# Kernel optimization log

Measured on AMD Instinct MI355X. Metric: run time of the kernel, lower is better.

The kernel has to match this reference:

```python
import jax, jax.numpy as jnp
import numpy as np

EMBED_DIM = 1024
NUM_HEADS = 16
HEAD_DIM = EMBED_DIM // NUM_HEADS
T_Q = 2048
T_K = 2048
B = 4
NEG_INF = -1e9


def setup_inputs() -> dict:
    key = jax.random.key(0)
    ks = jax.random.split(key, 8)
    q = jax.random.normal(ks[0], (T_Q, B, EMBED_DIM), dtype=jnp.float32)
    k = jax.random.normal(ks[1], (T_K, B, EMBED_DIM), dtype=jnp.float32)
    v = jax.random.normal(ks[2], (T_K, B, EMBED_DIM), dtype=jnp.float32)
    # True = padded key position (masked out)
    key_padding_mask = jax.random.randint(ks[3], (B, T_K), 0, 2).astype(jnp.bool_)
    # torch nn.Linear weights: shape (out, in), y = x @ W^T
    scale = 1.0 / np.sqrt(EMBED_DIM)
    Wq = jax.random.uniform(ks[4], (EMBED_DIM, EMBED_DIM), jnp.float32, -scale, scale)
    Wk = jax.random.uniform(ks[5], (EMBED_DIM, EMBED_DIM), jnp.float32, -scale, scale)
    Wv = jax.random.uniform(ks[6], (EMBED_DIM, EMBED_DIM), jnp.float32, -scale, scale)
    Wo = jax.random.uniform(ks[7], (EMBED_DIM, EMBED_DIM), jnp.float32, -scale, scale)
    return {"q": q, "k": k, "v": v, "key_padding_mask": key_padding_mask,
            "Wq": Wq, "Wk": Wk, "Wv": Wv, "Wo": Wo}


def _proj_split(W, x):
    # x: (T, B, E), W: (E, E) torch layout -> (B, H, T, d_k)
    T = x.shape[0]
    y = jnp.einsum('tbe,fe->tbf', x, W)
    return y.reshape(T, B, NUM_HEADS, HEAD_DIM).transpose(1, 2, 0, 3)


def reference(q, k, v, key_padding_mask, Wq, Wk, Wv, Wo):
    Q = _proj_split(Wq, q)  # (B, H, T_q, d_k)
    K = _proj_split(Wk, k)  # (B, H, T_k, d_k)
    V = _proj_split(Wv, v)  # (B, H, T_k, d_k)
    scores = jnp.einsum('bhqd,bhkd->bhqk', Q, K) / jnp.sqrt(
        jnp.asarray(HEAD_DIM, dtype=Q.dtype))
    scores = jnp.where(key_padding_mask[:, None, None, :], NEG_INF, scores)
    attn = jax.nn.softmax(scores, axis=-1)  # dropout p=0.0 -> identity
    out = jnp.einsum('bhqk,bhkd->bhqd', attn, V)  # (B, H, T_q, d_k)
    out = out.transpose(2, 0, 1, 3).reshape(q.shape[0], q.shape[1], EMBED_DIM)
    return jnp.einsum('tbe,fe->tbf', out, Wo)
```

## Files before the change

### kernel.cpp

```cpp
#include <hip/hip_runtime.h>
#include <stdint.h>

#define TSEQ 2048
#define NB   4
#define NH   16
#define HD   64
#define EMB  1024
#define ROWS (TSEQ*NB)
#define NKT  (EMB/64)
#define PREP_BLOCKS 28672

typedef __attribute__((ext_vector_type(8))) short bf16x8;
typedef __attribute__((ext_vector_type(4))) short bf16x4;
typedef __attribute__((ext_vector_type(4))) float f32x4;

__device__ __forceinline__ short f2bf(float x) {
    uint32_t u = __builtin_bit_cast(uint32_t, x);
    u += 0x7fffu + ((u >> 16) & 1u);
    return (short)(u >> 16);
}

__device__ __forceinline__ uint32_t pack2bf(float a, float b) {
    uint32_t ua = __builtin_bit_cast(uint32_t, a) + 0x8000u;
    uint32_t ub = __builtin_bit_cast(uint32_t, b) + 0x8000u;
    return (ua >> 16) | (ub & 0xffff0000u);
}

__device__ __forceinline__ void gld16(const void* g, void* l) {
    __builtin_amdgcn_global_load_lds(
        (const __attribute__((address_space(1))) void*)g,
        (__attribute__((address_space(3))) void*)l,
        16, 0, 0);
}

__global__ __launch_bounds__(256)
void prep_scan(const float* __restrict__ q, const float* __restrict__ k, const float* __restrict__ v,
               const float* __restrict__ Wq, const float* __restrict__ Wk,
               const float* __restrict__ Wv, const float* __restrict__ Wo,
               short* __restrict__ Wbf,
               short* __restrict__ Xq, short* __restrict__ Xk, short* __restrict__ Xv,
               const int* __restrict__ mask, int* __restrict__ idxc, int* __restrict__ inv,
               float* __restrict__ bias_c, int* __restrict__ npad)
{
    __shared__ int sums[256];
    __shared__ int totalv;
    const int bid = blockIdx.x, tid = threadIdx.x;

    if (bid < PREP_BLOCKS) {
        int gid = bid * 256 + tid;
        const float4* s4;
        bf16x4* d4;
        if (gid < (1 << 20)) {
            int wsel = gid >> 18;
            const float* src = (wsel == 0) ? Wq : (wsel == 1) ? Wk : (wsel == 2) ? Wv : Wo;
            s4 = (const float4*)src + (gid & ((1 << 18) - 1));
            d4 = (bf16x4*)Wbf + gid;
        } else {
            int iid = gid - (1 << 20);
            int isel = iid >> 21, o = iid & ((1 << 21) - 1);
            const float* src = (isel == 0) ? q : (isel == 1) ? k : v;
            short* dst = (isel == 0) ? Xq : (isel == 1) ? Xk : Xv;
            s4 = (const float4*)src + o;
            d4 = (bf16x4*)dst + o;
        }
        float4 vv = *s4;
        bf16x4 o4 = { f2bf(vv.x), f2bf(vv.y), f2bf(vv.z), f2bf(vv.w) };
        *d4 = o4;
        return;
    }

    const int b = bid - PREP_BLOCKS;
    const int* mb = mask + b * TSEQ;
    int valid[8]; int cnt = 0;
    #pragma unroll
    for (int j = 0; j < 8; j++) { valid[j] = (mb[tid * 8 + j] == 0); cnt += valid[j]; }
    sums[tid] = cnt;
    __syncthreads();
    for (int off = 1; off < 256; off <<= 1) {
        int vv = (tid >= off) ? sums[tid - off] : 0;
        __syncthreads();
        sums[tid] += vv;
        __syncthreads();
    }
    if (tid == 255) totalv = sums[255];
    int base = sums[tid] - cnt;
    __syncthreads();
    int nv = totalv;
    #pragma unroll
    for (int j = 0; j < 8; j++) {
        int t = tid * 8 + j;
        if (valid[j]) { idxc[b * TSEQ + base] = t; inv[b * TSEQ + t] = base; base++; }
        else          { inv[b * TSEQ + t] = -1; }
    }
    for (int i = tid; i < TSEQ; i += 256) {
        if (i >= nv) idxc[b * TSEQ + i] = 0;
        bias_c[b * TSEQ + i] = (i < nv) ? -12.0f : -1e9f;
    }
    if (tid == 0) npad[b] = (nv + 63) & ~63;
}


#define DSA(MH)                                                                     \
    _Pragma("unroll")                                                               \
    for (int mf = 0; mf < 4; mf++) {                                                \
        _Pragma("unroll")                                                           \
        for (int ks = 0; ks < 2; ks++) {                                            \
            const int rr = wm*64 + mf*16 + c;                                       \
            const int cb = (ks*64 + g*16) ^ ((rr & 7) << 4);                        \
            af[mf][ks] = *(const bf16x8*)(&lds[cur][0][MH][0] + rr*64 + (cb >> 1)); \
        }                                                                           \
    }

#define DSB(NH_, DST)                                                               \
    _Pragma("unroll")                                                               \
    for (int nf = 0; nf < 2; nf++) {                                                \
        _Pragma("unroll")                                                           \
        for (int ks = 0; ks < 2; ks++) {                                            \
            const int rr = wn*32 + nf*16 + c;                                       \
            const int cb = (ks*64 + g*16) ^ ((rr & 7) << 4);                        \
            DST[nf][ks] = *(const bf16x8*)(&lds[cur][1][NH_][0] + rr*64 + (cb >> 1));\
        }                                                                           \
    }

#define MM(MH, NH_, BREG)                                                           \
    __builtin_amdgcn_s_barrier();                                                   \
    asm volatile("s_waitcnt lgkmcnt(0)" ::: "memory");                              \
    __builtin_amdgcn_sched_barrier(0);                                              \
    __builtin_amdgcn_s_setprio(1);                                                  \
    _Pragma("unroll")                                                               \
    for (int mf = 0; mf < 4; mf++) {                                                \
        _Pragma("unroll")                                                           \
        for (int nf = 0; nf < 2; nf++) {                                            \
            acc[MH][NH_][mf][nf] = __builtin_amdgcn_mfma_f32_16x16x32_bf16(         \
                af[mf][0], BREG[nf][0], acc[MH][NH_][mf][nf], 0, 0, 0);             \
            acc[MH][NH_][mf][nf] = __builtin_amdgcn_mfma_f32_16x16x32_bf16(         \
                af[mf][1], BREG[nf][1], acc[MH][NH_][mf][nf], 0, 0, 0);             \
        }                                                                           \
    }                                                                               \
    __builtin_amdgcn_s_setprio(0);                                                  \
    __builtin_amdgcn_sched_barrier(0);

__global__ __launch_bounds__(512, 2)
void proj_gemm8(const short* __restrict__ Xq, const short* __restrict__ Xk, const short* __restrict__ Xv,
                const short* __restrict__ Wbf, const int* __restrict__ inv,
                short* __restrict__ Qw, short* __restrict__ Kc, short* __restrict__ Vw)
{
    __shared__ __align__(16) short lds[2][2][2][128*64];
    const int z = blockIdx.z;
    const short* __restrict__ A  = (z == 0) ? Xq : (z == 1) ? Xk : Xv;
    const short* __restrict__ Bw = Wbf + (size_t)z * (EMB*EMB);
    short* __restrict__ dst = (z == 0) ? Qw : (z == 1) ? Kc : Vw;
    const float scale = (z == 0) ? 0.18033688011112042f : 1.0f;

    const int tid = threadIdx.x;
    const int lane = tid & 63, w = tid >> 6;
    const int wm = w >> 2, wn = w & 3;
    const int g = lane >> 4, c = lane & 15;
    const int m0 = blockIdx.x * 256, n0 = blockIdx.y * 256;

    const short* a0 = A  + (size_t)m0 * EMB;
    const short* a1 = a0 + (size_t)128 * EMB;
    const short* b0 = Bw + (size_t)n0 * EMB;
    const short* b1 = b0 + (size_t)128 * EMB;

    auto stage = [&](const short* grow, short* lhalf) {
        #pragma unroll
        for (int p = 0; p < 2; p++) {
            const int lin = p * 8192 + w * 1024 + lane * 16;
            const int rin = lin >> 7;
            const int cb  = (lin & 127) ^ ((rin & 7) << 4);
            gld16(grow + (size_t)rin * EMB + (cb >> 1), lhalf + p * 4096 + w * 512);
        }
    };

    stage(a0,      &lds[0][0][0][0]);
    stage(a1,      &lds[0][0][1][0]);
    stage(b0,      &lds[0][1][0][0]);
    stage(b1,      &lds[0][1][1][0]);
    stage(a0 + 64, &lds[1][0][0][0]);
    stage(b0 + 64, &lds[1][1][0][0]);
    asm volatile("s_waitcnt vmcnt(4)" ::: "memory");
    __builtin_amdgcn_s_barrier();

    f32x4 acc[2][2][4][2] = {};

    #pragma unroll 2
    for (int t = 0; t < NKT; t++) {
        const int cur = t & 1, nxt = cur ^ 1;
        const int k1 = (t + 1 < NKT ? t + 1 : NKT - 1) * 64;
        const int k2 = (t + 2 < NKT ? t + 2 : NKT - 1) * 64;
        bf16x8 af[4][2], b0r[2][2], b1r[2][2];
        DSA(0); DSB(0, b0r);
        stage(a1 + k1, &lds[nxt][0][1][0]);
        MM(0, 0, b0r)
        __builtin_amdgcn_s_barrier();
        DSB(1, b1r);
        stage(b1 + k1, &lds[nxt][1][1][0]);
        MM(0, 1, b1r)
        __builtin_amdgcn_s_barrier();
        DSA(1);
        stage(a0 + k2, &lds[cur][0][0][0]);
        MM(1, 1, b1r)
        __builtin_amdgcn_s_barrier();
        stage(b0 + k2, &lds[cur][1][0][0]);
        MM(1, 0, b0r)
        asm volatile("s_waitcnt vmcnt(4)" ::: "memory");
        __builtin_amdgcn_s_barrier();
    }
    asm volatile("s_waitcnt vmcnt(0)" ::: "memory");

    if (z == 1) {
        #pragma unroll
        for (int mh = 0; mh < 2; mh++)
            #pragma unroll
            for (int nh = 0; nh < 2; nh++)
                #pragma unroll
                for (int mf = 0; mf < 4; mf++)
                    #pragma unroll
                    for (int nf = 0; nf < 2; nf++)
                        #pragma unroll
                        for (int r = 0; r < 4; r++) {
                            int row = m0 + mh*128 + wm*64 + mf*16 + g*4 + r;
                            int col = n0 + nh*128 + wn*32 + nf*16 + c;
                            int tq = row >> 2, bb = row & 3, h = col >> 6, dk = col & 63;
                            int i = inv[bb * TSEQ + tq];
                            if (i >= 0)
                                dst[(((size_t)(bb*16 + h) * TSEQ + i) << 6) + dk]
                                    = f2bf(acc[mh][nh][mf][nf][r]);
                        }
    } else {
        #pragma unroll
        for (int mh = 0; mh < 2; mh++)
            #pragma unroll
            for (int nh = 0; nh < 2; nh++)
                #pragma unroll
                for (int mf = 0; mf < 4; mf++)
                    #pragma unroll
                    for (int nf = 0; nf < 2; nf++)
                        #pragma unroll
                        for (int r = 0; r < 4; r++) {
                            int row = m0 + mh*128 + wm*64 + mf*16 + g*4 + r;
                            int col = n0 + nh*128 + wn*32 + nf*16 + c;
                            int tq = row >> 2, bb = row & 3, h = col >> 6, dk = col & 63;
                            dst[(((size_t)(bb*16 + h) * TSEQ + tq) << 6) + dk]
                                = f2bf(acc[mh][nh][mf][nf][r] * scale);
                        }
    }
}

__global__ __launch_bounds__(256)
void gather_v(const short* __restrict__ V,
              const int* __restrict__ idxc, const int* __restrict__ npad,
              short* __restrict__ Vtc)
{
    const int bh = blockIdx.y, b = bh >> 4;
    const int i0 = blockIdx.x * 64;
    if (i0 >= npad[b]) return;
    __shared__ __align__(16) short tile[64*72];
    __shared__ int sidx[64];
    const int tid = threadIdx.x;
    if (tid < 64) sidx[tid] = idxc[b * TSEQ + i0 + tid];
    __syncthreads();
    const short* __restrict__ Vh = V + (size_t)bh * TSEQ * HD;
    #pragma unroll
    for (int p = 0; p < 2; p++) {
        int idx = tid + p * 256, row = idx >> 3, cc = idx & 7;
        int src = sidx[row];
        *(int4*)(&tile[row * 72 + cc * 8]) = *(const int4*)(Vh + (size_t)src * HD + cc * 8);
    }
    __syncthreads();
    #pragma unroll
    for (int p = 0; p < 2; p++) {
        int idx = tid + p * 256, dv = idx >> 3, cc = idx & 7;
        bf16x8 o;
        #pragma unroll
        for (int j = 0; j < 8; j++) o[j] = tile[(cc * 8 + j) * 72 + dv];
        *(bf16x8*)(Vtc + ((size_t)bh * HD + dv) * TSEQ + i0 + cc * 8) = o;
    }
}

__global__ __launch_bounds__(256, 3)
void attn_kernel(const short* __restrict__ Q, const short* __restrict__ K,
                 const short* __restrict__ Vt, const float* __restrict__ bias,
                 const int* __restrict__ npad,
                 short* __restrict__ O)
{
    __shared__ __align__(16) short Ks [64*72];
    __shared__ __align__(16) short Vts[64*72];
    __shared__ __align__(16) short Ps [128*72];
    __shared__ __align__(16) float bias_lds[64];

    const int bh = blockIdx.y;
    const int b_ = bh >> 4, h_ = bh & 15;
    const int q0 = blockIdx.x * 128;
    const int tid = threadIdx.x, lane = tid & 63, wv = tid >> 6;
    const int g = lane >> 4, c = lane & 15;
    const int qb = wv * 32;
    const short* __restrict__ Qh  = Q  + (size_t)bh * TSEQ * HD;
    const short* __restrict__ Kh  = K  + (size_t)bh * TSEQ * HD;
    const short* __restrict__ Vth = Vt + (size_t)bh * HD * TSEQ;
    const float* __restrict__ biasb = bias + b_ * TSEQ;
    const int nit = npad[b_] >> 6;

    const int srow = tid >> 3, scc = tid & 7;

    *(int4*)(&Ks [ srow       * 72 + scc * 8]) = *(const int4*)(Kh  + (size_t) srow       * HD + scc * 8);
    *(int4*)(&Ks [(srow + 32) * 72 + scc * 8]) = *(const int4*)(Kh  + (size_t)(srow + 32) * HD + scc * 8);
    *(int4*)(&Vts[ srow       * 72 + scc * 8]) = *(const int4*)(Vth + (size_t) srow       * TSEQ + scc * 8);
    *(int4*)(&Vts[(srow + 32) * 72 + scc * 8]) = *(const int4*)(Vth + (size_t)(srow + 32) * TSEQ + scc * 8);
    if (tid < 16) ((float4*)bias_lds)[tid] = ((const float4*)biasb)[tid];

    bf16x8 qf[2][2];
    #pragma unroll
    for (int j = 0; j < 2; j++)
        #pragma unroll
        for (int ks = 0; ks < 2; ks++)
            qf[j][ks] = *(const bf16x8*)(Qh + (size_t)(q0 + qb + j * 16 + c) * HD + ks * 32 + g * 8);
    __syncthreads();

    float lacc[2] = { 0.0f, 0.0f };
    f32x4 oacc[2][4] = {};

    for (int it = 0; it < nit; it++) {
        f32x4 sacc[2][4];
        #pragma unroll
        for (int mt = 0; mt < 4; mt++) {
            f32x4 bv = *(const f32x4*)(&bias_lds[mt * 16 + g * 4]);
            sacc[0][mt] = bv; sacc[1][mt] = bv;
        }

        int4 kr0, kr1, vr0, vr1; float4 br;
        const bool pfv = (it + 1 < nit);
        if (pfv) {
            int tk0n = (it + 1) * 64;
            kr0 = *(const int4*)(Kh  + (size_t)(tk0n + srow)      * HD + scc * 8);
            kr1 = *(const int4*)(Kh  + (size_t)(tk0n + srow + 32) * HD + scc * 8);
            vr0 = *(const int4*)(Vth + (size_t) srow       * TSEQ + tk0n + scc * 8);
            vr1 = *(const int4*)(Vth + (size_t)(srow + 32) * TSEQ + tk0n + scc * 8);
            if (tid < 16) br = ((const float4*)(biasb + tk0n))[tid];
        }

        __builtin_amdgcn_s_setprio(1);
        #pragma unroll
        for (int ks = 0; ks < 2; ks++)
            #pragma unroll
            for (int mt = 0; mt < 4; mt++) {
                bf16x8 kf = *(const bf16x8*)(&Ks[(mt * 16 + c) * 72 + ks * 32 + g * 8]);
                sacc[0][mt] = __builtin_amdgcn_mfma_f32_16x16x32_bf16(kf, qf[0][ks], sacc[0][mt], 0, 0, 0);
                sacc[1][mt] = __builtin_amdgcn_mfma_f32_16x16x32_bf16(kf, qf[1][ks], sacc[1][mt], 0, 0, 0);
            }
        __builtin_amdgcn_s_setprio(0);

        #pragma unroll
        for (int j = 0; j < 2; j++) {
            int prow = (qb + j * 16 + c) * 72;
            float lp = 0.0f;
            #pragma unroll
            for (int mt = 0; mt < 4; mt++) {
                float e0 = __builtin_amdgcn_exp2f(sacc[j][mt][0]);
                float e1 = __builtin_amdgcn_exp2f(sacc[j][mt][1]);
                float e2 = __builtin_amdgcn_exp2f(sacc[j][mt][2]);
                float e3 = __builtin_amdgcn_exp2f(sacc[j][mt][3]);
                lp += (e0 + e1) + (e2 + e3);
                uint2 pw = { pack2bf(e0, e1), pack2bf(e2, e3) };
                *(uint2*)(&Ps[prow + mt * 16 + g * 4]) = pw;
            }
            lacc[j] += lp;
        }
        __builtin_amdgcn_sched_barrier(0);

        __builtin_amdgcn_s_setprio(1);
        #pragma unroll
        for (int s2 = 0; s2 < 2; s2++) {
            bf16x8 pf0 = *(const bf16x8*)(&Ps[(qb +      c) * 72 + s2 * 32 + g * 8]);
            bf16x8 pf1 = *(const bf16x8*)(&Ps[(qb + 16 + c) * 72 + s2 * 32 + g * 8]);
            #pragma unroll
            for (int mtv = 0; mtv < 4; mtv++) {
                bf16x8 vf = *(const bf16x8*)(&Vts[(mtv * 16 + c) * 72 + s2 * 32 + g * 8]);
                oacc[0][mtv] = __builtin_amdgcn_mfma_f32_16x16x32_bf16(vf, pf0, oacc[0][mtv], 0, 0, 0);
                oacc[1][mtv] = __builtin_amdgcn_mfma_f32_16x16x32_bf16(vf, pf1, oacc[1][mtv], 0, 0, 0);
            }
        }
        __builtin_amdgcn_s_setprio(0);

        if (pfv) {
            __syncthreads();
            *(int4*)(&Ks [ srow       * 72 + scc * 8]) = kr0;
            *(int4*)(&Ks [(srow + 32) * 72 + scc * 8]) = kr1;
            *(int4*)(&Vts[ srow       * 72 + scc * 8]) = vr0;
            *(int4*)(&Vts[(srow + 32) * 72 + scc * 8]) = vr1;
            if (tid < 16) ((float4*)bias_lds)[tid] = br;
            __syncthreads();
        }
    }

    __syncthreads();
    #pragma unroll
    for (int j = 0; j < 2; j++) {
        float l = lacc[j];
        l += __shfl_xor(l, 16);
        l += __shfl_xor(l, 32);
        float inv_ = 1.0f / l;
        int orow = (qb + j * 16 + c) * 72;
        #pragma unroll
        for (int mtv = 0; mtv < 4; mtv++) {
            uint2 ow = { pack2bf(oacc[j][mtv][0] * inv_, oacc[j][mtv][1] * inv_),
                         pack2bf(oacc[j][mtv][2] * inv_, oacc[j][mtv][3] * inv_) };
            *(uint2*)(&Ps[orow + mtv * 16 + g * 4]) = ow;
        }
    }
    __syncthreads();
    #pragma unroll
    for (int i = 0; i < 4; i++) {
        int idx = tid + i * 256, row = idx >> 3, cc = idx & 7;
        *(int4*)(O + (((size_t)(q0 + row) * NB + b_) << 10) + h_ * 64 + cc * 8)
            = *(const int4*)(&Ps[row * 72 + cc * 8]);
    }
}

__global__ __launch_bounds__(256, 2)
void out_gemm(const short* __restrict__ A, const short* __restrict__ Bw, float* __restrict__ C)
{
    __shared__ __align__(16) short As[128*32];
    __shared__ __align__(16) short Bs[128*32];
    const int tid = threadIdx.x;
    const int lane = tid & 63, w = tid >> 6;
    const int wm = w >> 1, wn = w & 1;
    const int g = lane >> 4, c = lane & 15;
    const int m0 = blockIdx.x * 128, n0 = blockIdx.y * 128;

    const int l4 = lane >> 2, col8 = (lane & 3) * 8;
    const short* gA = A  + (size_t)(m0 + w*16 + l4) * EMB + col8;
    const short* gB = Bw + (size_t)(n0 + w*16 + l4) * EMB + col8;
    short* ldsA0 = &As[(w*16) * 32];
    short* ldsA1 = &As[(64 + w*16) * 32];
    short* ldsB0 = &Bs[(w*16) * 32];
    short* ldsB1 = &Bs[(64 + w*16) * 32];

    f32x4 acc[4][4] = {};
    for (int kt = 0; kt < EMB; kt += 32) {
        gld16(gA + kt,          ldsA0);
        gld16(gA + 64*EMB + kt, ldsA1);
        gld16(gB + kt,          ldsB0);
        gld16(gB + 64*EMB + kt, ldsB1);
        __syncthreads();
        bf16x8 a[4], b[4];
        #pragma unroll
        for (int mt = 0; mt < 4; mt++) a[mt] = *(const bf16x8*)(&As[(wm*64 + mt*16 + c) * 32 + g * 8]);
        #pragma unroll
        for (int nt = 0; nt < 4; nt++) b[nt] = *(const bf16x8*)(&Bs[(wn*64 + nt*16 + c) * 32 + g * 8]);
        #pragma unroll
        for (int mt = 0; mt < 4; mt++)
            #pragma unroll
            for (int nt = 0; nt < 4; nt++)
                acc[mt][nt] = __builtin_amdgcn_mfma_f32_16x16x32_bf16(a[mt], b[nt], acc[mt][nt], 0, 0, 0);
        __syncthreads();
    }
    #pragma unroll
    for (int mt = 0; mt < 4; mt++)
        #pragma unroll
        for (int nt = 0; nt < 4; nt++)
            #pragma unroll
            for (int r = 0; r < 4; r++) {
                int row = m0 + wm*64 + mt*16 + g*4 + r;
                int col = n0 + wn*64 + nt*16 + c;
                C[(size_t)row * EMB + col] = acc[mt][nt][r];
            }
}

extern "C" void kernel_launch(void* const* d_in, const int* in_sizes, int n_in,
                              void* d_out, int out_size, void* d_ws, size_t ws_size,
                              hipStream_t stream)
{
    const float* q    = (const float*)d_in[0];
    const float* k    = (const float*)d_in[1];
    const float* v    = (const float*)d_in[2];
    const int*   mask = (const int*)  d_in[3];
    const float* Wq   = (const float*)d_in[4];
    const float* Wk   = (const float*)d_in[5];
    const float* Wv   = (const float*)d_in[6];
    const float* Wo   = (const float*)d_in[7];
    float* out = (float*)d_out;

    char* ws = (char*)d_ws;
    short* Wbf    = (short*)(ws);
    short* Qws    = (short*)(ws +  8388608);
    short* Kc     = (short*)(ws + 25165824);
    short* Vws    = (short*)(ws + 41943040);
    short* Vtc    = (short*)(ws + 58720256);
    short* Ows    = (short*)(ws + 75497472);
    float* bias_c = (float*)(ws + 92274688);
    short* Xvbf   = (short*)(ws + 92307456);
    int*   idxc   = (int*)  (ws + 109084672);
    int*   npad   = (int*)  (ws + 109117440);
    int*   inv    = (int*)  (ws + 109117504);
    short* Xqbf = Ows;
    short* Xkbf = Vtc;

    prep_scan<<<PREP_BLOCKS + NB, 256, 0, stream>>>(q, k, v, Wq, Wk, Wv, Wo,
                                                    Wbf, Xqbf, Xkbf, Xvbf,
                                                    mask, idxc, inv, bias_c, npad);
    proj_gemm8<<<dim3(ROWS/256, EMB/256, 3), 512, 0, stream>>>(Xqbf, Xkbf, Xvbf, Wbf, inv, Qws, Kc, Vws);
    gather_v<<<dim3(TSEQ/64, NB*NH), 256, 0, stream>>>(Vws, idxc, npad, Vtc);
    attn_kernel<<<dim3(TSEQ/128, NB*NH), 256, 0, stream>>>(Qws, Kc, Vtc, bias_c, npad, Ows);
    out_gemm<<<dim3(ROWS/128, EMB/128), 256, 0, stream>>>(Ows, Wbf + (size_t)3*EMB*EMB, out);
}
```

Before: 312.0 us.

## Gather unmasked key rows before K/V projection, write V transposed, drop gather_v

The K and V projections now load their input rows through the compacted index list, so each 256-row block covers only unmasked keys of one batch. Blocks lying wholly past the padded valid count exit early, which skips projection work for masked keys. The V projection epilogue writes straight into the transposed compacted layout, so the separate gather_v kernel and the inverse index map are removed. The cost is indirect row addressing in the A-operand loads and scattered 8-byte transposed stores for V.

```diff
diff --git a/kernel.cpp b/kernel.cpp
--- a/kernel.cpp
+++ b/kernel.cpp
@@ -39,7 +39,7 @@
                const float* __restrict__ Wv, const float* __restrict__ Wo,
                short* __restrict__ Wbf,
                short* __restrict__ Xq, short* __restrict__ Xk, short* __restrict__ Xv,
-               const int* __restrict__ mask, int* __restrict__ idxc, int* __restrict__ inv,
+               const int* __restrict__ mask, int* __restrict__ idxc,
                float* __restrict__ bias_c, int* __restrict__ npad)
 {
     __shared__ int sums[256];
@@ -87,11 +87,8 @@
     __syncthreads();
     int nv = totalv;
     #pragma unroll
-    for (int j = 0; j < 8; j++) {
-        int t = tid * 8 + j;
-        if (valid[j]) { idxc[b * TSEQ + base] = t; inv[b * TSEQ + t] = base; base++; }
-        else          { inv[b * TSEQ + t] = -1; }
-    }
+    for (int j = 0; j < 8; j++)
+        if (valid[j]) { idxc[b * TSEQ + base] = tid * 8 + j; base++; }
     for (int i = tid; i < TSEQ; i += 256) {
         if (i >= nv) idxc[b * TSEQ + i] = 0;
         bias_c[b * TSEQ + i] = (i < nv) ? -12.0f : -1e9f;
@@ -142,43 +139,61 @@
 
 __global__ __launch_bounds__(512, 2)
 void proj_gemm8(const short* __restrict__ Xq, const short* __restrict__ Xk, const short* __restrict__ Xv,
-                const short* __restrict__ Wbf, const int* __restrict__ inv,
-                short* __restrict__ Qw, short* __restrict__ Kc, short* __restrict__ Vw)
+                const short* __restrict__ Wbf,
+                const int* __restrict__ idxc, const int* __restrict__ npad,
+                short* __restrict__ Qw, short* __restrict__ Kc, short* __restrict__ Vt)
 {
+    const int z = blockIdx.z;
+    const int m0 = blockIdx.x * 256, n0 = blockIdx.y * 256;
+    const int bb0 = m0 >> 11;
+    if (z != 0 && (m0 & 2047) >= npad[bb0]) return;
+
     __shared__ __align__(16) short lds[2][2][2][128*64];
-    const int z = blockIdx.z;
     const short* __restrict__ A  = (z == 0) ? Xq : (z == 1) ? Xk : Xv;
     const short* __restrict__ Bw = Wbf + (size_t)z * (EMB*EMB);
-    short* __restrict__ dst = (z == 0) ? Qw : (z == 1) ? Kc : Vw;
-    const float scale = (z == 0) ? 0.18033688011112042f : 1.0f;
+    const float scale = 0.18033688011112042f;
 
     const int tid = threadIdx.x;
     const int lane = tid & 63, w = tid >> 6;
     const int wm = w >> 2, wn = w & 3;
     const int g = lane >> 4, c = lane & 15;
-    const int m0 = blockIdx.x * 256, n0 = blockIdx.y * 256;
-
-    const short* a0 = A  + (size_t)m0 * EMB;
-    const short* a1 = a0 + (size_t)128 * EMB;
-    const short* b0 = Bw + (size_t)n0 * EMB;
-    const short* b1 = b0 + (size_t)128 * EMB;
-
-    auto stage = [&](const short* grow, short* lhalf) {
+
+    int rin[2], swz[2], ldo[2];
+    #pragma unroll
+    for (int p = 0; p < 2; p++) {
+        const int lin = p * 8192 + w * 1024 + lane * 16;
+        rin[p] = lin >> 7;
+        swz[p] = ((lin & 127) ^ ((rin[p] & 7) << 4)) >> 1;
+        ldo[p] = p * 4096 + w * 512;
+    }
+    int aoff[2][2], boff[2][2];
+    #pragma unroll
+    for (int h = 0; h < 2; h++)
         #pragma unroll
         for (int p = 0; p < 2; p++) {
-            const int lin = p * 8192 + w * 1024 + lane * 16;
-            const int rin = lin >> 7;
-            const int cb  = (lin & 127) ^ ((rin & 7) << 4);
-            gld16(grow + (size_t)rin * EMB + (cb >> 1), lhalf + p * 4096 + w * 512);
-        }
+            if (z != 0) {
+                int t = idxc[bb0 * TSEQ + ((m0 & 2047) + h * 128 + rin[p])];
+                aoff[h][p] = (t * NB + bb0) * EMB + swz[p];
+            } else {
+                aoff[h][p] = (m0 + h * 128 + rin[p]) * EMB + swz[p];
+            }
+            boff[h][p] = (n0 + h * 128 + rin[p]) * EMB + swz[p];
+        }
+    auto stageA = [&](int h, int kt, short* lhalf) {
+        gld16(A + aoff[h][0] + kt, lhalf + ldo[0]);
+        gld16(A + aoff[h][1] + kt, lhalf + ldo[1]);
     };
-
-    stage(a0,      &lds[0][0][0][0]);
-    stage(a1,      &lds[0][0][1][0]);
-    stage(b0,      &lds[0][1][0][0]);
-    stage(b1,      &lds[0][1][1][0]);
-    stage(a0 + 64, &lds[1][0][0][0]);
-    stage(b0 + 64, &lds[1][1][0][0]);
+    auto stageB = [&](int h, int kt, short* lhalf) {
+        gld16(Bw + boff[h][0] + kt, lhalf + ldo[0]);
+        gld16(Bw + boff[h][1] + kt, lhalf + ldo[1]);
+    };
+
+    stageA(0, 0,  &lds[0][0][0][0]);
+    stageA(1, 0,  &lds[0][0][1][0]);
+    stageB(0, 0,  &lds[0][1][0][0]);
+    stageB(1, 0,  &lds[0][1][1][0]);
+    stageA(0, 64, &lds[1][0][0][0]);
+    stageB(0, 64, &lds[1][1][0][0]);
     asm volatile("s_waitcnt vmcnt(4)" ::: "memory");
     __builtin_amdgcn_s_barrier();
 
@@ -191,25 +206,25 @@
         const int k2 = (t + 2 < NKT ? t + 2 : NKT - 1) * 64;
         bf16x8 af[4][2], b0r[2][2], b1r[2][2];
         DSA(0); DSB(0, b0r);
-        stage(a1 + k1, &lds[nxt][0][1][0]);
+        stageA(1, k1, &lds[nxt][0][1][0]);
         MM(0, 0, b0r)
         __builtin_amdgcn_s_barrier();
         DSB(1, b1r);
-        stage(b1 + k1, &lds[nxt][1][1][0]);
+        stageB(1, k1, &lds[nxt][1][1][0]);
         MM(0, 1, b1r)
         __builtin_amdgcn_s_barrier();
         DSA(1);
-        stage(a0 + k2, &lds[cur][0][0][0]);
+        stageA(0, k2, &lds[cur][0][0][0]);
         MM(1, 1, b1r)
         __builtin_amdgcn_s_barrier();
-        stage(b0 + k2, &lds[cur][1][0][0]);
+        stageB(0, k2, &lds[cur][1][0][0]);
         MM(1, 0, b0r)
         asm volatile("s_waitcnt vmcnt(4)" ::: "memory");
         __builtin_amdgcn_s_barrier();
     }
     asm volatile("s_waitcnt vmcnt(0)" ::: "memory");
 
-    if (z == 1) {
+    if (z == 0) {
         #pragma unroll
         for (int mh = 0; mh < 2; mh++)
             #pragma unroll
@@ -223,12 +238,10 @@
                             int row = m0 + mh*128 + wm*64 + mf*16 + g*4 + r;
                             int col = n0 + nh*128 + wn*32 + nf*16 + c;
                             int tq = row >> 2, bb = row & 3, h = col >> 6, dk = col & 63;
-                            int i = inv[bb * TSEQ + tq];
-                            if (i >= 0)
-                                dst[(((size_t)(bb*16 + h) * TSEQ + i) << 6) + dk]
-                                    = f2bf(acc[mh][nh][mf][nf][r]);
+                            Qw[(((size_t)(bb*16 + h) * TSEQ + tq) << 6) + dk]
+                                = f2bf(acc[mh][nh][mf][nf][r] * scale);
                         }
-    } else {
+    } else if (z == 1) {
         #pragma unroll
         for (int mh = 0; mh < 2; mh++)
             #pragma unroll
@@ -241,41 +254,26 @@
                         for (int r = 0; r < 4; r++) {
                             int row = m0 + mh*128 + wm*64 + mf*16 + g*4 + r;
                             int col = n0 + nh*128 + wn*32 + nf*16 + c;
-                            int tq = row >> 2, bb = row & 3, h = col >> 6, dk = col & 63;
-                            dst[(((size_t)(bb*16 + h) * TSEQ + tq) << 6) + dk]
-                                = f2bf(acc[mh][nh][mf][nf][r] * scale);
+                            int i = row & 2047, bb = row >> 11, h = col >> 6, dk = col & 63;
+                            Kc[(((size_t)(bb*16 + h) * TSEQ + i) << 6) + dk]
+                                = f2bf(acc[mh][nh][mf][nf][r]);
                         }
-    }
-}
-
-__global__ __launch_bounds__(256)
-void gather_v(const short* __restrict__ V,
-              const int* __restrict__ idxc, const int* __restrict__ npad,
-              short* __restrict__ Vtc)
-{
-    const int bh = blockIdx.y, b = bh >> 4;
-    const int i0 = blockIdx.x * 64;
-    if (i0 >= npad[b]) return;
-    __shared__ __align__(16) short tile[64*72];
-    __shared__ int sidx[64];
-    const int tid = threadIdx.x;
-    if (tid < 64) sidx[tid] = idxc[b * TSEQ + i0 + tid];
-    __syncthreads();
-    const short* __restrict__ Vh = V + (size_t)bh * TSEQ * HD;
-    #pragma unroll
-    for (int p = 0; p < 2; p++) {
-        int idx = tid + p * 256, row = idx >> 3, cc = idx & 7;
-        int src = sidx[row];
-        *(int4*)(&tile[row * 72 + cc * 8]) = *(const int4*)(Vh + (size_t)src * HD + cc * 8);
-    }
-    __syncthreads();
-    #pragma unroll
-    for (int p = 0; p < 2; p++) {
-        int idx = tid + p * 256, dv = idx >> 3, cc = idx & 7;
-        bf16x8 o;
-        #pragma unroll
-        for (int j = 0; j < 8; j++) o[j] = tile[(cc * 8 + j) * 72 + dv];
-        *(bf16x8*)(Vtc + ((size_t)bh * HD + dv) * TSEQ + i0 + cc * 8) = o;
+    } else {
+        #pragma unroll
+        for (int mh = 0; mh < 2; mh++)
+            #pragma unroll
+            for (int nh = 0; nh < 2; nh++)
+                #pragma unroll
+                for (int mf = 0; mf < 4; mf++)
+                    #pragma unroll
+                    for (int nf = 0; nf < 2; nf++) {
+                        int row0 = m0 + mh*128 + wm*64 + mf*16 + g*4;
+                        int col  = n0 + nh*128 + wn*32 + nf*16 + c;
+                        int i0 = row0 & 2047, bb = row0 >> 11, h = col >> 6, dv = col & 63;
+                        bf16x4 o = { f2bf(acc[mh][nh][mf][nf][0]), f2bf(acc[mh][nh][mf][nf][1]),
+                                     f2bf(acc[mh][nh][mf][nf][2]), f2bf(acc[mh][nh][mf][nf][3]) };
+                        *(bf16x4*)(Vt + ((size_t)((bb*16 + h) * HD + dv) * TSEQ) + i0) = o;
+                    }
     }
 }
 
@@ -486,22 +484,20 @@
     short* Wbf    = (short*)(ws);
     short* Qws    = (short*)(ws +  8388608);
     short* Kc     = (short*)(ws + 25165824);
-    short* Vws    = (short*)(ws + 41943040);
+    short* Xkbf   = (short*)(ws + 41943040);
     short* Vtc    = (short*)(ws + 58720256);
     short* Ows    = (short*)(ws + 75497472);
     float* bias_c = (float*)(ws + 92274688);
     short* Xvbf   = (short*)(ws + 92307456);
     int*   idxc   = (int*)  (ws + 109084672);
     int*   npad   = (int*)  (ws + 109117440);
-    int*   inv    = (int*)  (ws + 109117504);
     short* Xqbf = Ows;
-    short* Xkbf = Vtc;
 
     prep_scan<<<PREP_BLOCKS + NB, 256, 0, stream>>>(q, k, v, Wq, Wk, Wv, Wo,
                                                     Wbf, Xqbf, Xkbf, Xvbf,
-                                                    mask, idxc, inv, bias_c, npad);
-    proj_gemm8<<<dim3(ROWS/256, EMB/256, 3), 512, 0, stream>>>(Xqbf, Xkbf, Xvbf, Wbf, inv, Qws, Kc, Vws);
-    gather_v<<<dim3(TSEQ/64, NB*NH), 256, 0, stream>>>(Vws, idxc, npad, Vtc);
+                                                    mask, idxc, bias_c, npad);
+    proj_gemm8<<<dim3(ROWS/256, EMB/256, 3), 512, 0, stream>>>(Xqbf, Xkbf, Xvbf, Wbf,
+                                                               idxc, npad, Qws, Kc, Vtc);
     attn_kernel<<<dim3(TSEQ/128, NB*NH), 256, 0, stream>>>(Qws, Kc, Vtc, bias_c, npad, Ows);
     out_gemm<<<dim3(ROWS/128, EMB/128), 256, 0, stream>>>(Ows, Wbf + (size_t)3*EMB*EMB, out);
 }
```

Result: no change. 307.5 us (-1.4%).
